# Optimization experiments

Measured on AMD Instinct MI355X. Metric: run time of the kernel, lower is better.

## Reference

```python
import jax, jax.numpy as jnp
import numpy as np
from jax import lax

EPS = 0.1
CHANNEL = 1


def _sobel_kernels(channel):
    # sobel: 3x3, each row [-0.5, 0, 0.5] -> varies along width (w)
    s = jnp.array([[-0.5, 0.0, 0.5],
                   [-0.5, 0.0, 0.5],
                   [-0.5, 0.0, 0.5]], dtype=jnp.float32)
    kx = jnp.broadcast_to(s, (3, 3, 3))          # [d,h,w], constant over d,h; torch sobel.repeat(c,1,3,1,1)
    ky = jnp.broadcast_to(s.T, (3, 3, 3))        # varies along h
    kz = jnp.stack([jnp.full((3, 3), -0.5, jnp.float32),
                    jnp.zeros((3, 3), jnp.float32),
                    jnp.full((3, 3), 0.5, jnp.float32)], axis=0)  # varies along d
    def rep(k):
        return jnp.tile(k[None, None], (channel, 1, 1, 1, 1))  # [C,1,3,3,3] OIDHW
    return rep(kx), rep(ky), rep(kz)


def _grad3(x_pad, kernel, channel):
    # x_pad: [N,C,D+2,H+2,W+2]; cross-correlation matching F.conv3d, padding=0
    return lax.conv_general_dilated(
        x_pad, kernel, window_strides=(1, 1, 1), padding='VALID',
        dimension_numbers=('NCDHW', 'OIDHW', 'NCDHW'),
        feature_group_count=channel)


def setup_inputs() -> dict:
    key = jax.random.key(0)
    k1, k2 = jax.random.split(key)
    shape = (1, 1, 192, 224, 192)
    I = jax.random.normal(k1, shape, dtype=jnp.float32)
    J = jax.random.normal(k2, shape, dtype=jnp.float32)
    return {"I": I, "J": J}


def reference(I, J):
    kx, ky, kz = _sobel_kernels(CHANNEL)
    pad = ((0, 0), (0, 0), (1, 1), (1, 1), (1, 1))
    I_pad = jnp.pad(I, pad, mode='edge')  # ReplicationPad3d(1)
    J_pad = jnp.pad(J, pad, mode='edge')
    Ix = _grad3(I_pad, kx, CHANNEL)
    Iy = _grad3(I_pad, ky, CHANNEL)
    Iz = _grad3(I_pad, kz, CHANNEL)
    Jx = _grad3(J_pad, kx, CHANNEL)
    Jy = _grad3(J_pad, ky, CHANNEL)
    Jz = _grad3(J_pad, kz, CHANNEL)
    I_mag = Ix * Ix + Iy * Iy + Iz * Iz + EPS * EPS
    J_mag = Jx * Jx + Jy * Jy + Jz * Jz + EPS * EPS
    dot = Ix * Jx + Iy * Jy + Iz * Jz  # == sum over concat channel dim (C=1)
    ngf = (dot * dot) / (I_mag * J_mag)
    return jnp.mean(1.0 - ngf)
```

## Files before the change

### kernel.cpp

```cpp
#include <hip/hip_runtime.h>
#include <stdint.h>

#define DD 192
#define HH 224
#define WW 192
#define PLANE (HH*WW)
#define TOTAL (DD*HH*WW)

#define HT 4
#define TROWS 6
#define DSEG 6
#define NSEG (DD/DSEG)
#define HTILES (HH/HT)
#define NT 256
#define NBLOCKS (HTILES*NSEG)

#define TILEF (TROWS*WW)
#define BUFF (2*TILEF)
#define NPIECE 576
#define GUARD 4

typedef __attribute__((address_space(3))) uint32_t lds_t;
typedef __attribute__((address_space(1))) const uint32_t glb_t;

#define BARRIER() asm volatile("s_barrier" ::: "memory")
#define WAITV3()  asm volatile("s_waitcnt vmcnt(3)" ::: "memory")
#define WAITV0()  asm volatile("s_waitcnt vmcnt(0)" ::: "memory")

struct PP {
    float IPT[3], IPS[3], IHD[3];
    float JPT[3], JPS[3], JHD[3];
};

__global__ __launch_bounds__(NT) void ngf_main_kernel(
    const float* __restrict__ I, const float* __restrict__ J,
    float* __restrict__ partial)
{
    __shared__ __align__(16) float lds[GUARD + 2 * BUFF + 4];
    const float EPS2 = 0.04f;

    int t    = threadIdx.x;
    int lane = t & 63;
    int w    = t >> 6;

    int bid0 = blockIdx.x;
    int bid  = (bid0 & 7) * (NBLOCKS / 8) + (bid0 >> 3);

    int th   = bid % HTILES;
    int seg  = bid / HTILES;
    int ds   = seg * DSEG;
    int hb   = th * HT;

    const float* sp[3];
    int lo[3];
    #pragma unroll
    for (int m = 0; m < 3; ++m) {
        int p = (m < 2) ? (t + m * NT) : (512 + lane);
        int inp = (p >= NPIECE / 2) ? 1 : 0;
        int q   = p - inp * (NPIECE / 2);
        int r   = q / 48, c = q % 48;
        int srow = min(max(hb - 1 + r, 0), HH - 1);
        sp[m] = (inp ? J : I) + srow * WW + c * 4;
        lo[m] = GUARD + 4 * p;
    }

    auto stage = [&](int dp, int buf) {
        size_t poff = (size_t)dp * PLANE;
        #pragma unroll
        for (int m = 0; m < 3; ++m) {
            __builtin_amdgcn_global_load_lds((glb_t*)(sp[m] + poff),
                (lds_t*)(&lds[buf * BUFF + lo[m]]), 16, 0, 0);
        }
    };

    int l3 = 3 * lane;
    bool b0  = (lane == 0);
    bool b63 = (lane == 63);

    auto combine = [&](int buf) -> PP {
        PP P;
        #pragma unroll
        for (int j = 0; j < 3; ++j) {
            P.IPT[j] = 0.f; P.IPS[j] = 0.f; P.IHD[j] = 0.f;
            P.JPT[j] = 0.f; P.JPS[j] = 0.f; P.JHD[j] = 0.f;
        }
        const float* base = &lds[GUARD + buf * BUFF];
        #pragma unroll
        for (int b = 0; b < 3; ++b) {
            const float* BI = base + (w + b) * WW;
            const float* BJ = BI + TILEF;
            {
                float Lr = BI[l3 - 1];
                float x0 = BI[l3], x1 = BI[l3 + 1], x2 = BI[l3 + 2];
                float Rr = BI[l3 + 3];
                float L = b0  ? x0 : Lr;
                float R = b63 ? x2 : Rr;
                float s0 = L  + x0 + x1;
                float s1 = x0 + x1 + x2;
                float s2 = x1 + x2 + R;
                P.IPT[0] += x1 - L;
                P.IPT[1] += x2 - x0;
                P.IPT[2] += R  - x1;
                P.IPS[0] += s0; P.IPS[1] += s1; P.IPS[2] += s2;
                if (b == 0) { P.IHD[0] -= s0; P.IHD[1] -= s1; P.IHD[2] -= s2; }
                if (b == 2) { P.IHD[0] += s0; P.IHD[1] += s1; P.IHD[2] += s2; }
            }
            {
                float Lr = BJ[l3 - 1];
                float x0 = BJ[l3], x1 = BJ[l3 + 1], x2 = BJ[l3 + 2];
                float Rr = BJ[l3 + 3];
                float L = b0  ? x0 : Lr;
                float R = b63 ? x2 : Rr;
                float s0 = L  + x0 + x1;
                float s1 = x0 + x1 + x2;
                float s2 = x1 + x2 + R;
                P.JPT[0] += x1 - L;
                P.JPT[1] += x2 - x0;
                P.JPT[2] += R  - x1;
                P.JPS[0] += s0; P.JPS[1] += s1; P.JPS[2] += s2;
                if (b == 0) { P.JHD[0] -= s0; P.JHD[1] -= s1; P.JHD[2] -= s2; }
                if (b == 2) { P.JHD[0] += s0; P.JHD[1] += s1; P.JHD[2] += s2; }
            }
        }
        return P;
    };

    auto dcl = [&](int m) { return min(max(ds + m, 0), DD - 1); };

    PP p[3];
    stage(dcl(-1), 0);
    stage(dcl(0), 1);
    WAITV3(); BARRIER();
    p[0] = combine(0);
    BARRIER();
    stage(dcl(1), 0);
    WAITV3(); BARRIER();
    p[1] = combine(1);
    BARRIER();
    stage(dcl(2), 1);

    float acc = 0.0f;
    #pragma unroll
    for (int k = 0; k < DSEG; ++k) {
        int buf = k & 1;
        if (k < DSEG - 1) { WAITV3(); }
        else             { WAITV0(); }
        BARRIER();

        __builtin_amdgcn_s_setprio(1);
        int sa = k % 3, sb2 = (k + 1) % 3, sc = (k + 2) % 3;
        p[sc] = combine(buf);

        #pragma unroll
        for (int j = 0; j < 3; ++j) {
            float Ix = p[sa].IPT[j] + p[sb2].IPT[j] + p[sc].IPT[j];
            float Iy = p[sa].IHD[j] + p[sb2].IHD[j] + p[sc].IHD[j];
            float Iz = p[sc].IPS[j] - p[sa].IPS[j];
            float Jx = p[sa].JPT[j] + p[sb2].JPT[j] + p[sc].JPT[j];
            float Jy = p[sa].JHD[j] + p[sb2].JHD[j] + p[sc].JHD[j];
            float Jz = p[sc].JPS[j] - p[sa].JPS[j];

            float Imag = fmaf(Ix, Ix, fmaf(Iy, Iy, fmaf(Iz, Iz, EPS2)));
            float Jmag = fmaf(Jx, Jx, fmaf(Jy, Jy, fmaf(Jz, Jz, EPS2)));
            float dot  = fmaf(Ix, Jx, fmaf(Iy, Jy, Iz * Jz));
            acc += 1.0f - (dot * dot) * __builtin_amdgcn_rcpf(Imag * Jmag);
        }
        __builtin_amdgcn_s_setprio(0);

        if (k < DSEG - 1) {
            BARRIER();
            if (k <= DSEG - 3)
                stage(dcl(k + 3), buf);
        }
    }

    #pragma unroll
    for (int o = 32; o > 0; o >>= 1)
        acc += __shfl_down(acc, o, 64);

    __shared__ float smem[NT / 64];
    if (lane == 0) smem[w] = acc;
    __syncthreads();
    if (t == 0)
        partial[bid] = smem[0] + smem[1] + smem[2] + smem[3];
}

__global__ __launch_bounds__(256) void ngf_reduce_kernel(
    const float* __restrict__ partial, float* __restrict__ out)
{
    double acc = 0.0;
    for (int i = threadIdx.x; i < NBLOCKS; i += blockDim.x)
        acc += (double)partial[i];

    #pragma unroll
    for (int o = 32; o > 0; o >>= 1)
        acc += __shfl_down(acc, o, 64);

    __shared__ double smem[4];
    int lane = threadIdx.x & 63;
    int wid  = threadIdx.x >> 6;
    if (lane == 0) smem[wid] = acc;
    __syncthreads();
    if (threadIdx.x == 0) {
        double s = smem[0] + smem[1] + smem[2] + smem[3];
        out[0] = (float)(s / (double)TOTAL);
    }
}

extern "C" void kernel_launch(void* const* d_in, const int* in_sizes, int n_in,
                              void* d_out, int out_size, void* d_ws, size_t ws_size,
                              hipStream_t stream)
{
    const float* I = (const float*)d_in[0];
    const float* J = (const float*)d_in[1];
    float* out = (float*)d_out;
    float* partial = (float*)d_ws;

    ngf_main_kernel<<<NBLOCKS, NT, 0, stream>>>(I, J, partial);
    ngf_reduce_kernel<<<1, 256, 0, stream>>>(partial, out);
}
```

Before: 29.90 us.

## Use single-wave blocks per output row to drop barriers and reorder staging

Blocks shrink from four waves covering four output rows to a single 64-lane wave covering one output row, so each block stages only three input rows per plane. This removes all s_barrier calls and the cross-wave LDS reduction; staging now waits on lgkmcnt before overwriting a buffer and is issued before the NGF arithmetic so loads overlap compute. The cost is halo reuse: each row is loaded three times instead of 1.5 times, so global and L2 traffic roughly doubles, and the grid now has four times as many small blocks.

Result: slower. 33.90 us (+13.4%).

```diff
diff --git a/kernel.cpp b/kernel.cpp
--- a/kernel.cpp
+++ b/kernel.cpp
@@ -7,25 +7,22 @@
 #define PLANE (HH*WW)
 #define TOTAL (DD*HH*WW)
 
-#define HT 4
-#define TROWS 6
 #define DSEG 6
 #define NSEG (DD/DSEG)
-#define HTILES (HH/HT)
-#define NT 256
-#define NBLOCKS (HTILES*NSEG)
-
-#define TILEF (TROWS*WW)
+#define NT 64
+#define NBLOCKS (HH*NSEG)
+
+#define TILEF (3*WW)
 #define BUFF (2*TILEF)
-#define NPIECE 576
+#define NPIECE 288
 #define GUARD 4
 
 typedef __attribute__((address_space(3))) uint32_t lds_t;
 typedef __attribute__((address_space(1))) const uint32_t glb_t;
 
-#define BARRIER() asm volatile("s_barrier" ::: "memory")
-#define WAITV3()  asm volatile("s_waitcnt vmcnt(3)" ::: "memory")
+#define WAITV5()  asm volatile("s_waitcnt vmcnt(5)" ::: "memory")
 #define WAITV0()  asm volatile("s_waitcnt vmcnt(0)" ::: "memory")
+#define LGKM0()   asm volatile("s_waitcnt lgkmcnt(0)" ::: "memory")
 
 struct PP {
     float IPT[3], IPS[3], IHD[3];
@@ -39,23 +36,21 @@
     __shared__ __align__(16) float lds[GUARD + 2 * BUFF + 4];
     const float EPS2 = 0.04f;
 
-    int t    = threadIdx.x;
-    int lane = t & 63;
-    int w    = t >> 6;
+    int lane = threadIdx.x;
 
     int bid0 = blockIdx.x;
     int bid  = (bid0 & 7) * (NBLOCKS / 8) + (bid0 >> 3);
 
-    int th   = bid % HTILES;
-    int seg  = bid / HTILES;
+    int hb   = bid % HH;
+    int seg  = bid / HH;
     int ds   = seg * DSEG;
-    int hb   = th * HT;
-
-    const float* sp[3];
-    int lo[3];
-    #pragma unroll
-    for (int m = 0; m < 3; ++m) {
-        int p = (m < 2) ? (t + m * NT) : (512 + lane);
+
+    const float* sp[5];
+    int lo[5];
+    #pragma unroll
+    for (int m = 0; m < 5; ++m) {
+        int p = lane + m * NT;
+        if (p >= NPIECE) p -= NPIECE;
         int inp = (p >= NPIECE / 2) ? 1 : 0;
         int q   = p - inp * (NPIECE / 2);
         int r   = q / 48, c = q % 48;
@@ -67,7 +62,7 @@
     auto stage = [&](int dp, int buf) {
         size_t poff = (size_t)dp * PLANE;
         #pragma unroll
-        for (int m = 0; m < 3; ++m) {
+        for (int m = 0; m < 5; ++m) {
             __builtin_amdgcn_global_load_lds((glb_t*)(sp[m] + poff),
                 (lds_t*)(&lds[buf * BUFF + lo[m]]), 16, 0, 0);
         }
@@ -87,7 +82,7 @@
         const float* base = &lds[GUARD + buf * BUFF];
         #pragma unroll
         for (int b = 0; b < 3; ++b) {
-            const float* BI = base + (w + b) * WW;
+            const float* BI = base + b * WW;
             const float* BJ = BI + TILEF;
             {
                 float Lr = BI[l3 - 1];
@@ -127,30 +122,11 @@
 
     auto dcl = [&](int m) { return min(max(ds + m, 0), DD - 1); };
 
+    float acc = 0.0f;
     PP p[3];
-    stage(dcl(-1), 0);
-    stage(dcl(0), 1);
-    WAITV3(); BARRIER();
-    p[0] = combine(0);
-    BARRIER();
-    stage(dcl(1), 0);
-    WAITV3(); BARRIER();
-    p[1] = combine(1);
-    BARRIER();
-    stage(dcl(2), 1);
-
-    float acc = 0.0f;
-    #pragma unroll
-    for (int k = 0; k < DSEG; ++k) {
-        int buf = k & 1;
-        if (k < DSEG - 1) { WAITV3(); }
-        else             { WAITV0(); }
-        BARRIER();
-
-        __builtin_amdgcn_s_setprio(1);
+
+    auto ngf = [&](int k) {
         int sa = k % 3, sb2 = (k + 1) % 3, sc = (k + 2) % 3;
-        p[sc] = combine(buf);
-
         #pragma unroll
         for (int j = 0; j < 3; ++j) {
             float Ix = p[sa].IPT[j] + p[sb2].IPT[j] + p[sc].IPT[j];
@@ -159,30 +135,46 @@
             float Jx = p[sa].JPT[j] + p[sb2].JPT[j] + p[sc].JPT[j];
             float Jy = p[sa].JHD[j] + p[sb2].JHD[j] + p[sc].JHD[j];
             float Jz = p[sc].JPS[j] - p[sa].JPS[j];
-
             float Imag = fmaf(Ix, Ix, fmaf(Iy, Iy, fmaf(Iz, Iz, EPS2)));
             float Jmag = fmaf(Jx, Jx, fmaf(Jy, Jy, fmaf(Jz, Jz, EPS2)));
             float dot  = fmaf(Ix, Jx, fmaf(Iy, Jy, Iz * Jz));
             acc += 1.0f - (dot * dot) * __builtin_amdgcn_rcpf(Imag * Jmag);
         }
+    };
+
+    stage(dcl(-1), 0);
+    stage(dcl(0), 1);
+    WAITV5();
+    p[0] = combine(0);
+    LGKM0();
+    stage(dcl(1), 0);
+    WAITV5();
+    p[1] = combine(1);
+    LGKM0();
+    stage(dcl(2), 1);
+
+    #pragma unroll
+    for (int k = 0; k < DSEG; ++k) {
+        int buf = k & 1;
+        if (k < DSEG - 1) { WAITV5(); }
+        else             { WAITV0(); }
+        __builtin_amdgcn_s_setprio(1);
+        p[(k + 2) % 3] = combine(buf);
         __builtin_amdgcn_s_setprio(0);
-
-        if (k < DSEG - 1) {
-            BARRIER();
-            if (k <= DSEG - 3)
-                stage(dcl(k + 3), buf);
-        }
+        if (k <= DSEG - 3) {
+            LGKM0();
+            stage(dcl(k + 3), buf);
+        }
+        __builtin_amdgcn_s_setprio(1);
+        ngf(k);
+        __builtin_amdgcn_s_setprio(0);
     }
 
     #pragma unroll
     for (int o = 32; o > 0; o >>= 1)
         acc += __shfl_down(acc, o, 64);
-
-    __shared__ float smem[NT / 64];
-    if (lane == 0) smem[w] = acc;
-    __syncthreads();
-    if (t == 0)
-        partial[bid] = smem[0] + smem[1] + smem[2] + smem[3];
+    if (lane == 0)
+        partial[bid] = acc;
 }
 
 __global__ __launch_bounds__(256) void ngf_reduce_kernel(
```
